# Performance work log

Hardware: AMD Instinct MI355X
Metric: run time of the kernel (lower is better)

The kernel has to match this reference:

```python
import jax, jax.numpy as jnp
import numpy as np

DIM = 768
NUM_HEADS = 12
HEAD_DIM = DIM // NUM_HEADS
SCALE = HEAD_DIM ** -0.5


def setup_inputs() -> dict:
    key = jax.random.key(0)
    ks = jax.random.split(key, 6)
    B, N, C = 4, 2048, DIM
    x = jax.random.normal(ks[0], (B, N, C), dtype=jnp.float32)
    qkv_weight = jax.random.normal(ks[1], (3 * C, C), dtype=jnp.float32) * (C ** -0.5)
    q_bias = jax.random.normal(ks[2], (C,), dtype=jnp.float32) * 0.02
    v_bias = jax.random.normal(ks[3], (C,), dtype=jnp.float32) * 0.02
    proj_weight = jax.random.normal(ks[4], (C, C), dtype=jnp.float32) * (C ** -0.5)
    proj_bias = jax.random.normal(ks[5], (C,), dtype=jnp.float32) * 0.02
    return {"x": x, "qkv_weight": qkv_weight, "q_bias": q_bias,
            "v_bias": v_bias, "proj_weight": proj_weight, "proj_bias": proj_bias}


def reference(x, qkv_weight, q_bias, v_bias, proj_weight, proj_bias):
    B, N, C = x.shape
    # bias = concat(q_bias, zeros_like(v_bias), v_bias)
    bias = jnp.concatenate([q_bias, jnp.zeros_like(v_bias), v_bias])
    qkv = x @ qkv_weight.T + bias                      # [B, N, 3C]
    qkv = qkv.reshape(B, N, 3, NUM_HEADS, HEAD_DIM)
    q, k, v = jnp.moveaxis(qkv, 2, 0)                  # each [B, N, H, hd]
    q = jnp.transpose(q, (0, 2, 1, 3)) * SCALE         # [B, H, N, hd]
    k = jnp.transpose(k, (0, 2, 1, 3))
    v = jnp.transpose(v, (0, 2, 1, 3))
    attn = jax.nn.softmax(jnp.einsum('bhqd,bhkd->bhqk', q, k), axis=-1)
    out = jnp.einsum('bhqk,bhkd->bhqd', attn, v)       # [B, H, N, hd]
    out = jnp.transpose(out, (0, 2, 1, 3)).reshape(B, N, C)
    return out @ proj_weight.T + proj_bias
```

## Files before the change

### kernel.cpp

```cpp
#include <hip/hip_runtime.h>
#include <cstdint>
#include <cstddef>

typedef _Float16 f16;
typedef _Float16 f16x8 __attribute__((ext_vector_type(8)));
typedef _Float16 f16x4 __attribute__((ext_vector_type(4)));
typedef __fp16 h16x2 __attribute__((ext_vector_type(2)));
typedef float f32x4 __attribute__((ext_vector_type(4)));

#define DIM 768
#define NHEAD 12
#define HD 64
#define BATCH 4
#define SEQ 2048
#define MROWS (BATCH*SEQ)
#define C3 (3*DIM)
#define NBH (BATCH*NHEAD)

__device__ __forceinline__ f32x4 mfma32(f16x8 a, f16x8 b, f32x4 c) {
  return __builtin_amdgcn_mfma_f32_16x16x32_f16(a, b, c, 0, 0, 0);
}
__device__ __forceinline__ f32x4 mfma16(f16x4 a, f16x4 b, f32x4 c) {
  return __builtin_amdgcn_mfma_f32_16x16x16f16(a, b, c, 0, 0, 0);
}

__device__ __forceinline__ void gl2lds16(const void* g, void* l) {
  __builtin_amdgcn_global_load_lds(
      (const __attribute__((address_space(1))) void*)g,
      (__attribute__((address_space(3))) void*)l, 16, 0, 0);
}

__global__ __launch_bounds__(256) void k_convert(
    const float* __restrict__ x, const float* __restrict__ wqkv,
    const float* __restrict__ wproj,
    f16* __restrict__ xh, f16* __restrict__ wqh, f16* __restrict__ wph)
{
  const int NX = MROWS*DIM/4, NW = C3*DIM/4;
  int i = blockIdx.x * 256 + threadIdx.x;
  const float4* src; f16* dst; int idx;
  if (i < NX)         { src = (const float4*)x;     dst = xh;  idx = i; }
  else if (i < NX+NW) { src = (const float4*)wqkv;  dst = wqh; idx = i - NX; }
  else                { src = (const float4*)wproj; dst = wph; idx = i - NX - NW; }
  float4 v = src[idx];
  union { f16 h[4]; uint64_t u; } r;
  r.h[0] = (f16)v.x; r.h[1] = (f16)v.y; r.h[2] = (f16)v.z; r.h[3] = (f16)v.w;
  ((uint64_t*)dst)[idx] = r.u;
}

__device__ __forceinline__ void gemm_tile(
    const f16* __restrict__ A, const f16* __restrict__ B,
    int lda, int ldb, int K, int m0, int n0,
    f16* smem, f32x4 acc[4][4])
{
  f16* sA0 = smem;          f16* sA1 = smem + 8192;
  f16* sB0 = smem + 16384;  f16* sB1 = smem + 24576;
  const int tid = threadIdx.x, wid = tid >> 6;
  const int lane = tid & 63, lane15 = lane & 15, quad = lane >> 4;
  const int wm = wid >> 1, wn = wid & 1;

  auto stage = [&](int k0, f16* sA, f16* sB) {
    #pragma unroll
    for (int i = 0; i < 4; i++) {
      int j = i*256 + tid;
      int row = j >> 3;
      int sc  = (j & 7) ^ (row & 7);
      gl2lds16(A + (size_t)(m0 + row)*lda + k0 + sc*8, sA + (i*256 + wid*64)*8);
      gl2lds16(B + (size_t)(n0 + row)*ldb + k0 + sc*8, sB + (i*256 + wid*64)*8);
    }
  };

  const int NK = K >> 6;
  stage(0, sA0, sB0);
  for (int kk = 0; kk < NK; kk++) {
    f16* cA = (kk & 1) ? sA1 : sA0;
    f16* cB = (kk & 1) ? sB1 : sB0;
    __syncthreads();
    if (kk + 1 < NK)
      stage((kk + 1) << 6, (kk & 1) ? sA0 : sA1, (kk & 1) ? sB0 : sB1);
    #pragma unroll
    for (int ks = 0; ks < 2; ks++) {
      f16x8 af[4], bf[4];
      #pragma unroll
      for (int t = 0; t < 4; t++) {
        int ra = wm*64 + t*16 + lane15;
        af[t] = *(const f16x8*)(cA + ra*64 + (((ks*4 + quad) ^ (ra & 7)) << 3));
        int rb = wn*64 + t*16 + lane15;
        bf[t] = *(const f16x8*)(cB + rb*64 + (((ks*4 + quad) ^ (rb & 7)) << 3));
      }
      #pragma unroll
      for (int mt = 0; mt < 4; mt++)
        #pragma unroll
        for (int nt = 0; nt < 4; nt++)
          acc[mt][nt] = mfma32(af[mt], bf[nt], acc[mt][nt]);
    }
  }
}

__global__ __launch_bounds__(256, 2) void k_qkv(
    const f16* __restrict__ xh, const f16* __restrict__ wqh,
    const float* __restrict__ q_bias, const float* __restrict__ v_bias,
    f16* __restrict__ Qh, f16* __restrict__ Kh, f16* __restrict__ Vt)
{
  __shared__ f16 smem[32768];
  f32x4 acc[4][4];
  const f32x4 z4 = {0.f, 0.f, 0.f, 0.f};
  #pragma unroll
  for (int a = 0; a < 4; a++)
    #pragma unroll
    for (int b = 0; b < 4; b++) acc[a][b] = z4;

  const int m0 = blockIdx.y * 128, n0 = blockIdx.x * 128;
  gemm_tile(xh, wqh, DIM, DIM, DIM, m0, n0, smem, acc);

  const int tid = threadIdx.x, wid = tid >> 6, lane = tid & 63;
  const int lane15 = lane & 15, quad = lane >> 4;
  const int wm = wid >> 1, wn = wid & 1;
  const int bb = m0 >> 11, nbase = m0 & (SEQ - 1);
  const float QS = 0.125f * 1.4426950408889634f;

  f16* sT = smem;
  __syncthreads();

  if (n0 < 2*DIM) {
    const bool isQ = (n0 < DIM);
    #pragma unroll
    for (int nt = 0; nt < 4; nt++) {
      int col_l = wn*64 + nt*16 + lane15;
      int col = n0 + col_l;
      float b = isQ ? q_bias[col] : 0.f;
      #pragma unroll
      for (int mt = 0; mt < 4; mt++)
        #pragma unroll
        for (int r = 0; r < 4; r++) {
          int m_l = wm*64 + mt*16 + quad*4 + r;
          float v = acc[mt][nt][r] + b;
          if (isQ) v *= QS;
          sT[m_l*136 + col_l] = (f16)v;
        }
    }
    __syncthreads();
    #pragma unroll
    for (int it = 0; it < 8; it++) {
      int idx = it*256 + tid;
      int m_l = idx >> 4, ch = idx & 15;
      f16x8 val = *(const f16x8*)(sT + m_l*136 + ch*8);
      int col = n0 + ch*8;
      int c2 = isQ ? col : (col - DIM);
      int h = c2 >> 6, d = c2 & 63;
      f16* dst = isQ ? Qh : Kh;
      *(f16x8*)(dst + (((size_t)(bb*NHEAD + h)*SEQ + nbase + m_l) << 6) + d) = val;
    }
  } else {
    #pragma unroll
    for (int nt = 0; nt < 4; nt++) {
      int col_l = wn*64 + nt*16 + lane15;
      int c2 = n0 - 2*DIM + col_l;
      float b = v_bias[c2];
      #pragma unroll
      for (int mt = 0; mt < 4; mt++)
        #pragma unroll
        for (int r = 0; r < 4; r++) {
          int m_l = wm*64 + mt*16 + quad*4 + r;
          sT[col_l*136 + m_l] = (f16)(acc[mt][nt][r] + b);
        }
    }
    __syncthreads();
    #pragma unroll
    for (int it = 0; it < 8; it++) {
      int idx = it*256 + tid;
      int d_l = idx >> 4, m8 = idx & 15;
      f16x8 val = *(const f16x8*)(sT + d_l*136 + m8*8);
      int c2 = n0 - 2*DIM + d_l;
      int h = c2 >> 6, d = c2 & 63;
      *(f16x8*)(Vt + ((size_t)(bb*NHEAD + h)*HD + d)*SEQ + nbase + m8*8) = val;
    }
  }
}

#define KVT 128
#define NIT (SEQ/KVT)
__global__ __launch_bounds__(256, 3) void k_attn(
    const f16* __restrict__ Qh, const f16* __restrict__ Kh,
    const f16* __restrict__ Vt, f16* __restrict__ attnh)
{
  __shared__ f16 smem[2*8192 + 64*132];
  f16* sK0 = smem;
  f16* sK1 = smem + 8192;
  f16* sV  = smem + 16384;

  const int tid = threadIdx.x, wid = tid >> 6, lane = tid & 63;
  const int lane15 = lane & 15, quad = lane >> 4;
  const int q0 = blockIdx.x * 128;
  const int bh = blockIdx.y;
  const int qw = q0 + wid*32;

  const f16* Kbh = Kh + (size_t)bh*SEQ*HD;
  const f16* Vbh = Vt + (size_t)bh*HD*SEQ;

  f16x8 qf[2][2];
  #pragma unroll
  for (int qt = 0; qt < 2; qt++)
    #pragma unroll
    for (int ks = 0; ks < 2; ks++)
      qf[qt][ks] = *(const f16x8*)(Qh + ((size_t)bh*SEQ + qw + qt*16 + lane15)*HD
                                      + ks*32 + quad*8);

  f32x4 o[4][2];
  f32x4 sacc[2];
  const f32x4 z4 = {0.f, 0.f, 0.f, 0.f};
  #pragma unroll
  for (int dt = 0; dt < 4; dt++)
    #pragma unroll
    for (int qt = 0; qt < 2; qt++) o[dt][qt] = z4;
  sacc[0] = z4; sacc[1] = z4;
  const f16x4 one4 = {(f16)1.f, (f16)1.f, (f16)1.f, (f16)1.f};

  const int vrow = tid >> 2, vcg = (tid & 3) * 32;
  const f16* vsrc = Vbh + (size_t)vrow*SEQ + vcg;

  auto stageK = [&](int kv0, f16* sK) {
    #pragma unroll
    for (int i = 0; i < 4; i++) {
      int j = i*256 + tid;
      int row = j >> 3;
      int sc  = (j & 7) ^ (row & 7);
      gl2lds16(Kbh + (size_t)(kv0 + row)*HD + sc*8, sK + (i*256 + wid*64)*8);
    }
  };

  stageK(0, sK0);
  f16x8 vreg[4];
  #pragma unroll
  for (int j = 0; j < 4; j++) vreg[j] = *(const f16x8*)(vsrc + j*8);

  for (int it = 0; it < NIT; it++) {
    f16* cK = (it & 1) ? sK1 : sK0;
    __syncthreads();
    #pragma unroll
    for (int j = 0; j < 4; j++) {
      union { f16x8 v; f16x4 h[2]; } u; u.v = vreg[j];
      *(f16x4*)(sV + vrow*132 + vcg + j*8)     = u.h[0];
      *(f16x4*)(sV + vrow*132 + vcg + j*8 + 4) = u.h[1];
    }
    __syncthreads();
    if (it + 1 < NIT) {
      stageK((it + 1)*KVT, (it & 1) ? sK0 : sK1);
      #pragma unroll
      for (int j = 0; j < 4; j++)
        vreg[j] = *(const f16x8*)(vsrc + (it + 1)*KVT + j*8);
    }

    #pragma unroll
    for (int c = 0; c < 4; c++) {
      f16x8 ka[2][2];
      #pragma unroll
      for (int kt = 0; kt < 2; kt++) {
        int rb = c*32 + kt*16 + lane15;
        #pragma unroll
        for (int ks = 0; ks < 2; ks++)
          ka[ks][kt] = *(const f16x8*)(cK + rb*64 + (((ks*4 + quad) ^ (rb & 7)) << 3));
      }
      f32x4 s[2][2];
      #pragma unroll
      for (int kt = 0; kt < 2; kt++)
        #pragma unroll
        for (int qt = 0; qt < 2; qt++) s[kt][qt] = z4;
      #pragma unroll
      for (int ks = 0; ks < 2; ks++)
        #pragma unroll
        for (int kt = 0; kt < 2; kt++)
          #pragma unroll
          for (int qt = 0; qt < 2; qt++)
            s[kt][qt] = mfma32(ka[ks][kt], qf[qt][ks], s[kt][qt]);

      f16x4 pb[2][2];
      #pragma unroll
      for (int kt = 0; kt < 2; kt++)
        #pragma unroll
        for (int qt = 0; qt < 2; qt++) {
          union { h16x2 g2[2]; f16x4 h4; } u;
          u.g2[0] = __builtin_amdgcn_cvt_pkrtz(exp2f(s[kt][qt][0]), exp2f(s[kt][qt][1]));
          u.g2[1] = __builtin_amdgcn_cvt_pkrtz(exp2f(s[kt][qt][2]), exp2f(s[kt][qt][3]));
          pb[kt][qt] = u.h4;
        }
      #pragma unroll
      for (int kt = 0; kt < 2; kt++)
        #pragma unroll
        for (int qt = 0; qt < 2; qt++)
          sacc[qt] = mfma16(one4, pb[kt][qt], sacc[qt]);

      #pragma unroll
      for (int dt = 0; dt < 4; dt++) {
        int row = dt*16 + lane15;
        #pragma unroll
        for (int kt = 0; kt < 2; kt++) {
          int c16 = 4*c + 2*kt + (quad >> 1);
          f16x4 va = *(const f16x4*)(sV + row*132 + c16*8 + (quad & 1)*4);
          #pragma unroll
          for (int qt = 0; qt < 2; qt++)
            o[dt][qt] = mfma16(va, pb[kt][qt], o[dt][qt]);
        }
      }
    }
  }

  float inv[2] = {1.f / sacc[0][0], 1.f / sacc[1][0]};

  __syncthreads();
  f16* tb = smem + wid * (32 * 72);
  #pragma unroll
  for (int dt = 0; dt < 4; dt++)
    #pragma unroll
    for (int qt = 0; qt < 2; qt++) {
      f32x4 v = o[dt][qt];
      float iv = inv[qt];
      f16x4 hx = {(f16)(v[0]*iv), (f16)(v[1]*iv), (f16)(v[2]*iv), (f16)(v[3]*iv)};
      *(f16x4*)(tb + (qt*16 + lane15)*72 + dt*16 + quad*4) = hx;
    }
  __syncthreads();
  const int b = bh / NHEAD, h = bh % NHEAD;
  #pragma unroll
  for (int i = 0; i < 4; i++) {
    int row = i*8 + (lane >> 3);
    f16x8 rv = *(const f16x8*)(tb + row*72 + (lane & 7)*8);
    *(f16x8*)(attnh + ((size_t)b*SEQ + qw + row)*DIM + h*HD + (lane & 7)*8) = rv;
  }
}

__global__ __launch_bounds__(256, 2) void k_proj(
    const f16* __restrict__ ah, const f16* __restrict__ wph,
    const float* __restrict__ pbias, float* __restrict__ out)
{
  __shared__ f16 smem[32768];
  f32x4 acc[4][4];
  const f32x4 z4 = {0.f, 0.f, 0.f, 0.f};
  #pragma unroll
  for (int a = 0; a < 4; a++)
    #pragma unroll
    for (int b = 0; b < 4; b++) acc[a][b] = z4;

  const int m0 = blockIdx.y * 128, n0 = blockIdx.x * 128;
  gemm_tile(ah, wph, DIM, DIM, DIM, m0, n0, smem, acc);

  const int tid = threadIdx.x, wid = tid >> 6, lane = tid & 63;
  const int lane15 = lane & 15, quad = lane >> 4;
  const int wm = wid >> 1, wn = wid & 1;
  #pragma unroll
  for (int nt = 0; nt < 4; nt++) {
    int col = n0 + wn*64 + nt*16 + lane15;
    float bias = pbias[col];
    #pragma unroll
    for (int mt = 0; mt < 4; mt++) {
      #pragma unroll
      for (int r = 0; r < 4; r++) {
        int m = m0 + wm*64 + mt*16 + quad*4 + r;
        out[(size_t)m*DIM + col] = acc[mt][nt][r] + bias;
      }
    }
  }
}

extern "C" void kernel_launch(void* const* d_in, const int* in_sizes, int n_in,
                              void* d_out, int out_size, void* d_ws, size_t ws_size,
                              hipStream_t stream) {
  const float* x    = (const float*)d_in[0];
  const float* wqkv = (const float*)d_in[1];
  const float* qb   = (const float*)d_in[2];
  const float* vb   = (const float*)d_in[3];
  const float* wp   = (const float*)d_in[4];
  const float* pb   = (const float*)d_in[5];
  float* out = (float*)d_out;

  f16* p = (f16*)d_ws;
  f16* xh  = p; p += (size_t)MROWS*DIM;
  f16* wqh = p; p += (size_t)C3*DIM;
  f16* wph = p; p += (size_t)DIM*DIM;
  f16* Qh  = p; p += (size_t)NBH*SEQ*HD;
  f16* Kh  = p; p += (size_t)NBH*SEQ*HD;
  f16* Vt  = p; p += (size_t)NBH*SEQ*HD;
  f16* attnh = xh;

  k_convert<<<8448, 256, 0, stream>>>(x, wqkv, wp, xh, wqh, wph);
  k_qkv<<<dim3(C3/128, MROWS/128), 256, 0, stream>>>(xh, wqh, qb, vb, Qh, Kh, Vt);
  k_attn<<<dim3(SEQ/128, NBH), 256, 0, stream>>>(Qh, Kh, Vt, attnh);
  k_proj<<<dim3(DIM/128, MROWS/128), 256, 0, stream>>>(attnh, wph, pb, out);
}
```

Baseline: 236.4 us.

## Halve GEMM K-tile, swap operands to write outputs directly without LDS transpose

The shared GEMM tile now stages a 32-wide K slice instead of 64, halving LDS use so launch bounds rise to four blocks per CU. For Q/K and the projection, the weight and activation operands are swapped, so each lane's accumulator holds four consecutive feature columns and can be stored as a vector straight to global memory. This removes the LDS transpose and its extra barriers. The projection grid is also reordered so row blocks vary fastest. The trade-off is more K iterations and barriers per tile, and narrower 8-byte or 16-byte scattered stores instead of coalesced 16-byte row writes.

```diff
diff --git a/kernel.cpp b/kernel.cpp
--- a/kernel.cpp
+++ b/kernel.cpp
@@ -49,130 +49,112 @@
 
 __device__ __forceinline__ void gemm_tile(
     const f16* __restrict__ A, const f16* __restrict__ B,
-    int lda, int ldb, int K, int m0, int n0,
+    int lda, int ldb, int K, int am0, int bn0,
     f16* smem, f32x4 acc[4][4])
 {
-  f16* sA0 = smem;          f16* sA1 = smem + 8192;
-  f16* sB0 = smem + 16384;  f16* sB1 = smem + 24576;
+  f16* sA0 = smem;         f16* sA1 = smem + 4096;
+  f16* sB0 = smem + 8192;  f16* sB1 = smem + 12288;
   const int tid = threadIdx.x, wid = tid >> 6;
   const int lane = tid & 63, lane15 = lane & 15, quad = lane >> 4;
   const int wm = wid >> 1, wn = wid & 1;
 
   auto stage = [&](int k0, f16* sA, f16* sB) {
     #pragma unroll
-    for (int i = 0; i < 4; i++) {
+    for (int i = 0; i < 2; i++) {
       int j = i*256 + tid;
-      int row = j >> 3;
-      int sc  = (j & 7) ^ (row & 7);
-      gl2lds16(A + (size_t)(m0 + row)*lda + k0 + sc*8, sA + (i*256 + wid*64)*8);
-      gl2lds16(B + (size_t)(n0 + row)*ldb + k0 + sc*8, sB + (i*256 + wid*64)*8);
+      int row = j >> 2;
+      int sc  = (j & 3) ^ ((row >> 1) & 3);
+      gl2lds16(A + (size_t)(am0 + row)*lda + k0 + sc*8, sA + (i*256 + wid*64)*8);
+      gl2lds16(B + (size_t)(bn0 + row)*ldb + k0 + sc*8, sB + (i*256 + wid*64)*8);
     }
   };
 
-  const int NK = K >> 6;
+  const int NK = K >> 5;
   stage(0, sA0, sB0);
   for (int kk = 0; kk < NK; kk++) {
     f16* cA = (kk & 1) ? sA1 : sA0;
     f16* cB = (kk & 1) ? sB1 : sB0;
     __syncthreads();
     if (kk + 1 < NK)
-      stage((kk + 1) << 6, (kk & 1) ? sA0 : sA1, (kk & 1) ? sB0 : sB1);
-    #pragma unroll
-    for (int ks = 0; ks < 2; ks++) {
-      f16x8 af[4], bf[4];
-      #pragma unroll
-      for (int t = 0; t < 4; t++) {
-        int ra = wm*64 + t*16 + lane15;
-        af[t] = *(const f16x8*)(cA + ra*64 + (((ks*4 + quad) ^ (ra & 7)) << 3));
-        int rb = wn*64 + t*16 + lane15;
-        bf[t] = *(const f16x8*)(cB + rb*64 + (((ks*4 + quad) ^ (rb & 7)) << 3));
-      }
-      #pragma unroll
-      for (int mt = 0; mt < 4; mt++)
-        #pragma unroll
-        for (int nt = 0; nt < 4; nt++)
-          acc[mt][nt] = mfma32(af[mt], bf[nt], acc[mt][nt]);
-    }
-  }
-}
-
-__global__ __launch_bounds__(256, 2) void k_qkv(
+      stage((kk + 1) << 5, (kk & 1) ? sA0 : sA1, (kk & 1) ? sB0 : sB1);
+    f16x8 af[4], bf[4];
+    #pragma unroll
+    for (int t = 0; t < 4; t++) {
+      int ra = wm*64 + t*16 + lane15;
+      af[t] = *(const f16x8*)(cA + ra*32 + ((quad ^ ((ra >> 1) & 3)) << 3));
+      int rb = wn*64 + t*16 + lane15;
+      bf[t] = *(const f16x8*)(cB + rb*32 + ((quad ^ ((rb >> 1) & 3)) << 3));
+    }
+    #pragma unroll
+    for (int mt = 0; mt < 4; mt++)
+      #pragma unroll
+      for (int nt = 0; nt < 4; nt++)
+        acc[mt][nt] = mfma32(af[mt], bf[nt], acc[mt][nt]);
+  }
+}
+
+__global__ __launch_bounds__(256, 4) void k_qkv(
     const f16* __restrict__ xh, const f16* __restrict__ wqh,
     const float* __restrict__ q_bias, const float* __restrict__ v_bias,
     f16* __restrict__ Qh, f16* __restrict__ Kh, f16* __restrict__ Vt)
 {
-  __shared__ f16 smem[32768];
+  __shared__ f16 smem[16384];
   f32x4 acc[4][4];
   const f32x4 z4 = {0.f, 0.f, 0.f, 0.f};
   #pragma unroll
   for (int a = 0; a < 4; a++)
     #pragma unroll
     for (int b = 0; b < 4; b++) acc[a][b] = z4;
-
-  const int m0 = blockIdx.y * 128, n0 = blockIdx.x * 128;
-  gemm_tile(xh, wqh, DIM, DIM, DIM, m0, n0, smem, acc);
 
   const int tid = threadIdx.x, wid = tid >> 6, lane = tid & 63;
   const int lane15 = lane & 15, quad = lane >> 4;
   const int wm = wid >> 1, wn = wid & 1;
-  const int bb = m0 >> 11, nbase = m0 & (SEQ - 1);
+  const int cblk = blockIdx.x * 128;
+  const int mblk = blockIdx.y * 128;
+  const int bb = mblk >> 11, nbase = mblk & (SEQ - 1);
   const float QS = 0.125f * 1.4426950408889634f;
 
-  f16* sT = smem;
-  __syncthreads();
-
-  if (n0 < 2*DIM) {
-    const bool isQ = (n0 < DIM);
+  if (cblk < 2*DIM) {
+    gemm_tile(wqh, xh, DIM, DIM, DIM, cblk, mblk, smem, acc);
+    const bool isQ = (cblk < DIM);
+    #pragma unroll
+    for (int mt = 0; mt < 4; mt++) {
+      int c0 = cblk + wm*64 + mt*16 + quad*4;
+      int cr = isQ ? c0 : (c0 - DIM);
+      int h = cr >> 6, d0 = cr & 63;
+      float4 qb4 = isQ ? *(const float4*)(q_bias + c0) : make_float4(0,0,0,0);
+      f16* dst = isQ ? Qh : Kh;
+      f16* base = dst + (((size_t)(bb*NHEAD + h)*SEQ + nbase) << 6) + d0;
+      #pragma unroll
+      for (int nt = 0; nt < 4; nt++) {
+        int n = wn*64 + nt*16 + lane15;
+        f32x4 v = acc[mt][nt];
+        f16x4 hv;
+        if (isQ) {
+          hv[0] = (f16)((v[0] + qb4.x) * QS); hv[1] = (f16)((v[1] + qb4.y) * QS);
+          hv[2] = (f16)((v[2] + qb4.z) * QS); hv[3] = (f16)((v[3] + qb4.w) * QS);
+        } else {
+          hv[0] = (f16)v[0]; hv[1] = (f16)v[1]; hv[2] = (f16)v[2]; hv[3] = (f16)v[3];
+        }
+        *(f16x4*)(base + ((size_t)n << 6)) = hv;
+      }
+    }
+  } else {
+    gemm_tile(xh, wqh, DIM, DIM, DIM, mblk, cblk, smem, acc);
     #pragma unroll
     for (int nt = 0; nt < 4; nt++) {
-      int col_l = wn*64 + nt*16 + lane15;
-      int col = n0 + col_l;
-      float b = isQ ? q_bias[col] : 0.f;
-      #pragma unroll
-      for (int mt = 0; mt < 4; mt++)
-        #pragma unroll
-        for (int r = 0; r < 4; r++) {
-          int m_l = wm*64 + mt*16 + quad*4 + r;
-          float v = acc[mt][nt][r] + b;
-          if (isQ) v *= QS;
-          sT[m_l*136 + col_l] = (f16)v;
-        }
-    }
-    __syncthreads();
-    #pragma unroll
-    for (int it = 0; it < 8; it++) {
-      int idx = it*256 + tid;
-      int m_l = idx >> 4, ch = idx & 15;
-      f16x8 val = *(const f16x8*)(sT + m_l*136 + ch*8);
-      int col = n0 + ch*8;
-      int c2 = isQ ? col : (col - DIM);
+      int c = cblk + wn*64 + nt*16 + lane15;
+      int c2 = c - 2*DIM;
       int h = c2 >> 6, d = c2 & 63;
-      f16* dst = isQ ? Qh : Kh;
-      *(f16x8*)(dst + (((size_t)(bb*NHEAD + h)*SEQ + nbase + m_l) << 6) + d) = val;
-    }
-  } else {
-    #pragma unroll
-    for (int nt = 0; nt < 4; nt++) {
-      int col_l = wn*64 + nt*16 + lane15;
-      int c2 = n0 - 2*DIM + col_l;
       float b = v_bias[c2];
-      #pragma unroll
-      for (int mt = 0; mt < 4; mt++)
-        #pragma unroll
-        for (int r = 0; r < 4; r++) {
-          int m_l = wm*64 + mt*16 + quad*4 + r;
-          sT[col_l*136 + m_l] = (f16)(acc[mt][nt][r] + b);
-        }
-    }
-    __syncthreads();
-    #pragma unroll
-    for (int it = 0; it < 8; it++) {
-      int idx = it*256 + tid;
-      int d_l = idx >> 4, m8 = idx & 15;
-      f16x8 val = *(const f16x8*)(sT + d_l*136 + m8*8);
-      int c2 = n0 - 2*DIM + d_l;
-      int h = c2 >> 6, d = c2 & 63;
-      *(f16x8*)(Vt + ((size_t)(bb*NHEAD + h)*HD + d)*SEQ + nbase + m8*8) = val;
+      f16* base = Vt + ((size_t)(bb*NHEAD + h)*HD + d)*SEQ + nbase;
+      #pragma unroll
+      for (int mt = 0; mt < 4; mt++) {
+        int n0 = wm*64 + mt*16 + quad*4;
+        f32x4 v = acc[mt][nt];
+        f16x4 hv = {(f16)(v[0]+b), (f16)(v[1]+b), (f16)(v[2]+b), (f16)(v[3]+b)};
+        *(f16x4*)(base + n0) = hv;
+      }
     }
   }
 }
@@ -327,11 +309,11 @@
   }
 }
 
-__global__ __launch_bounds__(256, 2) void k_proj(
+__global__ __launch_bounds__(256, 4) void k_proj(
     const f16* __restrict__ ah, const f16* __restrict__ wph,
     const float* __restrict__ pbias, float* __restrict__ out)
 {
-  __shared__ f16 smem[32768];
+  __shared__ f16 smem[16384];
   f32x4 acc[4][4];
   const f32x4 z4 = {0.f, 0.f, 0.f, 0.f};
   #pragma unroll
@@ -339,23 +321,23 @@
     #pragma unroll
     for (int b = 0; b < 4; b++) acc[a][b] = z4;
 
-  const int m0 = blockIdx.y * 128, n0 = blockIdx.x * 128;
-  gemm_tile(ah, wph, DIM, DIM, DIM, m0, n0, smem, acc);
+  const int cblk = blockIdx.y * 128;
+  const int mblk = blockIdx.x * 128;
+  gemm_tile(wph, ah, DIM, DIM, DIM, cblk, mblk, smem, acc);
 
   const int tid = threadIdx.x, wid = tid >> 6, lane = tid & 63;
   const int lane15 = lane & 15, quad = lane >> 4;
   const int wm = wid >> 1, wn = wid & 1;
   #pragma unroll
-  for (int nt = 0; nt < 4; nt++) {
-    int col = n0 + wn*64 + nt*16 + lane15;
-    float bias = pbias[col];
-    #pragma unroll
-    for (int mt = 0; mt < 4; mt++) {
-      #pragma unroll
-      for (int r = 0; r < 4; r++) {
-        int m = m0 + wm*64 + mt*16 + quad*4 + r;
-        out[(size_t)m*DIM + col] = acc[mt][nt][r] + bias;
-      }
+  for (int mt = 0; mt < 4; mt++) {
+    int c0 = cblk + wm*64 + mt*16 + quad*4;
+    float4 b4 = *(const float4*)(pbias + c0);
+    #pragma unroll
+    for (int nt = 0; nt < 4; nt++) {
+      int m = mblk + wn*64 + nt*16 + lane15;
+      f32x4 v = acc[mt][nt];
+      float4 r = make_float4(v[0]+b4.x, v[1]+b4.y, v[2]+b4.z, v[3]+b4.w);
+      *(float4*)(out + (size_t)m*DIM + c0) = r;
     }
   }
 }
@@ -383,5 +365,5 @@
   k_convert<<<8448, 256, 0, stream>>>(x, wqkv, wp, xh, wqh, wph);
   k_qkv<<<dim3(C3/128, MROWS/128), 256, 0, stream>>>(xh, wqh, qb, vb, Qh, Kh, Vt);
   k_attn<<<dim3(SEQ/128, NBH), 256, 0, stream>>>(Qh, Kh, Vt, attnh);
-  k_proj<<<dim3(DIM/128, MROWS/128), 256, 0, stream>>>(attnh, wph, pb, out);
-}
+  k_proj<<<dim3(MROWS/128, DIM/128), 256, 0, stream>>>(attnh, wph, pb, out);
+}
```

New measurement: 235.5 us. About the same (-0.4%).
